# Kernel tuning notes

Measured on AMD Instinct MI355X. Metric: run time of the kernel, lower is better.

The kernel has to match this reference:

```python
import jax, jax.numpy as jnp
import numpy as np

N_NODES = 50000
N_EDGES = 1600000
IN_FEATS = 256
OUT_FEATS = 64


def setup_inputs() -> dict:
    key = jax.random.key(0)
    k_x, k_w, k_b, k_s, k_d = jax.random.split(key, 5)
    x = jax.random.normal(k_x, (N_NODES, IN_FEATS), dtype=jnp.float32)
    # nn.Linear(in_feats, out_feats): weight [out, in], bias [out]
    W = jax.random.normal(k_w, (OUT_FEATS, IN_FEATS), dtype=jnp.float32) / np.sqrt(IN_FEATS)
    b = jax.random.normal(k_b, (OUT_FEATS,), dtype=jnp.float32) * 0.01
    edge_src = jax.random.randint(k_s, (N_EDGES,), 0, N_NODES, dtype=jnp.int32)
    edge_dst = jax.random.randint(k_d, (N_EDGES,), 0, N_NODES, dtype=jnp.int32)
    return {"x": x, "W": W, "b": b, "edge_src": edge_src, "edge_dst": edge_dst}


def reference(x, W, b, edge_src, edge_dst):
    # h = dropout(relu(Linear(x)))  -- dropout p=0 (eval) => identity
    h = jax.nn.relu(x @ W.T + b)                     # [N, out_feats]
    # update_all: message = h[src], reduce = mean over incoming edges per dst
    msg = h[edge_src]                                # [E, out_feats] gather
    summed = jax.ops.segment_sum(msg, edge_dst, num_segments=N_NODES)  # [N, out]
    deg = jax.ops.segment_sum(jnp.ones((edge_src.shape[0],), dtype=h.dtype),
                              edge_dst, num_segments=N_NODES)          # [N]
    deg = jnp.maximum(deg, 1.0)
    return summed / deg[:, None]
```

## Files before the change

### kernel.cpp

```cpp
#include <hip/hip_runtime.h>
#include <hip/hip_bf16.h>

#define K_IN 256
#define O_OUT 64
#define NBINS 1024
#define NPB 49
#define CAP 1824
#define PART_CHUNK 4096
#define WS_STRIDE 264
#define XS_STRIDE 136

typedef __attribute__((ext_vector_type(8))) short short8;
typedef __attribute__((ext_vector_type(4))) float f32x4;

__device__ inline unsigned short bf16bits(float a) {
  __hip_bfloat16 t = __float2bfloat16(a);
  return *(unsigned short*)&t;
}

__global__ __launch_bounds__(256) void k_prep(const float* __restrict__ W,
                                              unsigned short* __restrict__ Wb,
                                              int* __restrict__ cursor) {
  int i = blockIdx.x * 256 + threadIdx.x;
  Wb[i] = bf16bits(W[i]);
  if (i < NBINS) cursor[i] = 0;
}

__global__ __launch_bounds__(256) void k_gemm_mfma(const float* __restrict__ x,
                                                   const unsigned short* __restrict__ Wb,
                                                   const float* __restrict__ bias,
                                                   __hip_bfloat16* __restrict__ h,
                                                   int N) {
  __shared__ unsigned short wsb[64 * WS_STRIDE];
  __shared__ unsigned short xs[64 * XS_STRIDE];

  const int tid = threadIdx.x;
  const int lane = tid & 63;
  const int wv = tid >> 6;
  const int n0 = blockIdx.x * 64;

  {
    const unsigned* wsrc = (const unsigned*)Wb;
    unsigned* wdst = (unsigned*)wsb;
#pragma unroll
    for (int r = 0; r < 32; ++r) {
      int flat = r * 256 + tid;
      int row = flat >> 7;
      int col = flat & 127;
      wdst[row * (WS_STRIDE / 2) + col] = wsrc[flat];
    }
  }

  f32x4 acc[4] = {{0.f, 0.f, 0.f, 0.f}, {0.f, 0.f, 0.f, 0.f},
                  {0.f, 0.f, 0.f, 0.f}, {0.f, 0.f, 0.f, 0.f}};

  for (int kc = 0; kc < K_IN; kc += 128) {
    __syncthreads();
    unsigned* xdst = (unsigned*)xs;
#pragma unroll
    for (int r = 0; r < 8; ++r) {
      int flat = r * 256 + tid;
      int row = flat >> 5;
      int c4 = flat & 31;
      float4 v = make_float4(0.f, 0.f, 0.f, 0.f);
      int node = n0 + row;
      if (node < N) v = *(const float4*)(x + (size_t)node * K_IN + kc + c4 * 4);
      unsigned u0 = (unsigned)bf16bits(v.x) | ((unsigned)bf16bits(v.y) << 16);
      unsigned u1 = (unsigned)bf16bits(v.z) | ((unsigned)bf16bits(v.w) << 16);
      xdst[row * (XS_STRIDE / 2) + c4 * 2] = u0;
      xdst[row * (XS_STRIDE / 2) + c4 * 2 + 1] = u1;
    }
    __syncthreads();

    const unsigned short* arow =
        xs + (wv * 16 + (lane & 15)) * XS_STRIDE + (lane >> 4) * 8;
    const unsigned short* bcol =
        wsb + (lane & 15) * WS_STRIDE + kc + (lane >> 4) * 8;
#pragma unroll
    for (int k0 = 0; k0 < 128; k0 += 32) {
      short8 a = *(const short8*)(arow + k0);
#pragma unroll
      for (int nt = 0; nt < 4; ++nt) {
        short8 bfr = *(const short8*)(bcol + nt * 16 * WS_STRIDE + k0);
        acc[nt] = __builtin_amdgcn_mfma_f32_16x16x32_bf16(a, bfr, acc[nt], 0, 0, 0);
      }
    }
  }

  const int col = lane & 15;
  const int rbase = (lane >> 4) * 4;
#pragma unroll
  for (int nt = 0; nt < 4; ++nt) {
    float bv = bias[nt * 16 + col];
#pragma unroll
    for (int j = 0; j < 4; ++j) {
      int node = n0 + wv * 16 + rbase + j;
      if (node < N) {
        float v = fmaxf(acc[nt][j] + bv, 0.f);
        h[(size_t)node * O_OUT + nt * 16 + col] = __float2bfloat16(v);
      }
    }
  }
}

__global__ __launch_bounds__(256) void k_part(const int* __restrict__ esrc,
                                              const int* __restrict__ edst,
                                              int* __restrict__ cursor,
                                              unsigned* __restrict__ bucket, int E) {
  __shared__ int cnt[NBINS];
  __shared__ int scanb[NBINS];
  __shared__ int gbase[NBINS];
  __shared__ int wsum[4];
  __shared__ unsigned ord[PART_CHUNK];
  __shared__ unsigned short obin[PART_CHUNK];

  const int tid = threadIdx.x;
  const int lane = tid & 63;
  const int wid = tid >> 6;
  const int base = blockIdx.x * PART_CHUNK;

#pragma unroll
  for (int r = 0; r < 4; ++r) cnt[r * 256 + tid] = 0;
  __syncthreads();

  unsigned pk[16];
  int bn[16];
  int rk[16];
#pragma unroll
  for (int r = 0; r < 4; ++r) {
    int e0 = base + r * 1024 + tid * 4;
    int4 s4, d4;
    if (e0 + 3 < E) {
      s4 = *(const int4*)(esrc + e0);
      d4 = *(const int4*)(edst + e0);
    } else {
      s4 = make_int4(0, 0, 0, 0);
      d4 = make_int4(0, 0, 0, 0);
      int* sp = (int*)&s4;
      int* dp = (int*)&d4;
      for (int j = 0; j < 4; ++j)
        if (e0 + j < E) { sp[j] = esrc[e0 + j]; dp[j] = edst[e0 + j]; }
    }
    const int* sp = (const int*)&s4;
    const int* dp = (const int*)&d4;
#pragma unroll
    for (int j = 0; j < 4; ++j) {
      int k = r * 4 + j;
      int e = e0 + j;
      if (e < E) {
        int s = sp[j];
        int d = dp[j];
        int bb = (int)__umulhi((unsigned)d, 87652394u);
        int dl = d - bb * NPB;
        pk[k] = (unsigned)s | ((unsigned)dl << 16);
        bn[k] = bb;
        rk[k] = atomicAdd(&cnt[bb], 1);
      } else {
        bn[k] = -1;
      }
    }
  }
  __syncthreads();

  int c0 = cnt[4 * tid];
  int c1 = cnt[4 * tid + 1];
  int c2 = cnt[4 * tid + 2];
  int c3 = cnt[4 * tid + 3];
  int s = c0 + c1 + c2 + c3;
  int incl = s;
#pragma unroll
  for (int off = 1; off < 64; off <<= 1) {
    int t = __shfl_up(incl, off);
    if (lane >= off) incl += t;
  }
  if (lane == 63) wsum[wid] = incl;
  __syncthreads();
  int wpre = 0;
  for (int w = 0; w < wid; ++w) wpre += wsum[w];
  int excl = wpre + incl - s;
  scanb[4 * tid] = excl;
  scanb[4 * tid + 1] = excl + c0;
  scanb[4 * tid + 2] = excl + c0 + c1;
  scanb[4 * tid + 3] = excl + c0 + c1 + c2;
  gbase[4 * tid] = (c0 > 0) ? atomicAdd(&cursor[4 * tid], c0) : 0;
  gbase[4 * tid + 1] = (c1 > 0) ? atomicAdd(&cursor[4 * tid + 1], c1) : 0;
  gbase[4 * tid + 2] = (c2 > 0) ? atomicAdd(&cursor[4 * tid + 2], c2) : 0;
  gbase[4 * tid + 3] = (c3 > 0) ? atomicAdd(&cursor[4 * tid + 3], c3) : 0;
  __syncthreads();

#pragma unroll
  for (int k = 0; k < 16; ++k) {
    if (bn[k] >= 0) {
      int pos = scanb[bn[k]] + rk[k];
      ord[pos] = pk[k];
      obin[pos] = (unsigned short)bn[k];
    }
  }
  __syncthreads();

  int nv = E - base;
  if (nv > PART_CHUNK) nv = PART_CHUNK;
  for (int p = tid; p < nv; p += 256) {
    int bb = obin[p];
    int slot = gbase[bb] + (p - scanb[bb]);
    if (slot < CAP) bucket[(size_t)bb * CAP + slot] = ord[p];
  }
}

__global__ __launch_bounds__(512) void k_sortagg(const unsigned* __restrict__ bucket,
                                                 const int* __restrict__ cursor,
                                                 const unsigned* __restrict__ h32,
                                                 float* __restrict__ out, int N) {
  __shared__ int hist[NPB];
  __shared__ int offs[NPB];
  __shared__ unsigned short sbuf[CAP];

  const int tid = threadIdx.x;
  const int lane = tid & 63;
  const int wid = tid >> 6;
  const int bin = blockIdx.x;

  if (tid < NPB) hist[tid] = 0;
  __syncthreads();

  int cnt = cursor[bin];
  if (cnt > CAP) cnt = CAP;
  const unsigned* bb = bucket + (size_t)bin * CAP;

  unsigned pk[4];
  int rk[4];
  {
    int i0 = tid * 4;
    uint4 v;
    if (i0 + 3 < cnt) {
      v = *(const uint4*)(bb + i0);
    } else {
      v = make_uint4(0, 0, 0, 0);
      unsigned* vp = (unsigned*)&v;
      for (int j = 0; j < 4; ++j)
        if (i0 + j < cnt) vp[j] = bb[i0 + j];
    }
    const unsigned* vp = (const unsigned*)&v;
#pragma unroll
    for (int j = 0; j < 4; ++j) {
      if (i0 + j < cnt) {
        pk[j] = vp[j];
        rk[j] = atomicAdd(&hist[vp[j] >> 16], 1);
      } else {
        rk[j] = -1;
      }
    }
  }
  __syncthreads();

  if (tid < 64) {
    int hval = (tid < NPB) ? hist[tid] : 0;
    int incl = hval;
#pragma unroll
    for (int off = 1; off < 64; off <<= 1) {
      int t = __shfl_up(incl, off);
      if (lane >= off) incl += t;
    }
    if (tid < NPB) offs[tid] = incl - hval;
  }
  __syncthreads();

#pragma unroll
  for (int j = 0; j < 4; ++j) {
    if (rk[j] >= 0) sbuf[offs[pk[j] >> 16] + rk[j]] = (unsigned short)(pk[j] & 0xFFFFu);
  }
  __syncthreads();

  const int half = lane >> 5;
  const int hl = lane & 31;
  for (int nl = wid; nl < NPB; nl += 8) {
    int n = bin * NPB + nl;
    if (n >= N) break;
    int c = hist[nl];
    const unsigned short* bs = sbuf + offs[nl];

    float ax = 0.f, ay = 0.f;
    const int npairs = c >> 1;
    const int g8 = npairs & ~7;
    if (g8 > 0) {
      int p[8];
#pragma unroll
      for (int k = 0; k < 8; ++k) p[k] = bs[2 * k + half];
      for (int i = 8;; i += 8) {
        int q[8];
        bool more = (i < g8);
        if (more) {
#pragma unroll
          for (int k = 0; k < 8; ++k) q[k] = bs[2 * (i + k) + half];
        }
#pragma unroll
        for (int k = 0; k < 8; ++k) {
          unsigned u = h32[(size_t)p[k] * 32 + hl];
          ax += __uint_as_float(u << 16);
          ay += __uint_as_float(u & 0xFFFF0000u);
        }
        if (!more) break;
#pragma unroll
        for (int k = 0; k < 8; ++k) p[k] = q[k];
      }
    }
    for (int j = g8; j < npairs; ++j) {
      int p = bs[2 * j + half];
      unsigned u = h32[(size_t)p * 32 + hl];
      ax += __uint_as_float(u << 16);
      ay += __uint_as_float(u & 0xFFFF0000u);
    }
    if (c & 1) {
      int p = bs[c - 1];
      if (half == 0) {
        unsigned u = h32[(size_t)p * 32 + hl];
        ax += __uint_as_float(u << 16);
        ay += __uint_as_float(u & 0xFFFF0000u);
      }
    }

    float bx = __shfl(ax, lane ^ 32);
    float by = __shfl(ay, lane ^ 32);
    if (half == 0) {
      float inv = 1.f / fmaxf((float)c, 1.f);
      float2 r;
      r.x = (ax + bx) * inv;
      r.y = (ay + by) * inv;
      ((float2*)out)[(size_t)n * 32 + hl] = r;
    }
  }
}

extern "C" void kernel_launch(void* const* d_in, const int* in_sizes, int n_in,
                              void* d_out, int out_size, void* d_ws, size_t ws_size,
                              hipStream_t stream) {
  const float* x = (const float*)d_in[0];
  const float* W = (const float*)d_in[1];
  const float* b = (const float*)d_in[2];
  const int* esrc = (const int*)d_in[3];
  const int* edst = (const int*)d_in[4];
  float* out = (float*)d_out;

  const int N = in_sizes[0] / K_IN;
  const int E = in_sizes[3];

  char* ws = (char*)d_ws;
  unsigned short* Wb = (unsigned short*)ws;
  __hip_bfloat16* h = (__hip_bfloat16*)(ws + 32768);
  size_t off = 32768 + (size_t)N * O_OUT * sizeof(__hip_bfloat16);
  int* cursor = (int*)(ws + off);
  off += NBINS * sizeof(int);
  unsigned* bucket = (unsigned*)(ws + off);

  k_prep<<<(K_IN * O_OUT) / 256, 256, 0, stream>>>(W, Wb, cursor);
  k_gemm_mfma<<<(N + 63) / 64, 256, 0, stream>>>(x, Wb, b, h, N);
  k_part<<<(E + PART_CHUNK - 1) / PART_CHUNK, 256, 0, stream>>>(esrc, edst, cursor, bucket, E);
  k_sortagg<<<NBINS, 512, 0, stream>>>(bucket, cursor, (const unsigned*)h, out, N);
}
```

Measured before the change: 176.9 us.

## Fuse GEMM and edge partition kernels into one interleaved launch

Merges the MFMA linear+ReLU kernel and the edge partitioning kernel into a single launch. Blocks are interleaved so that every third block does partitioning and the rest do GEMM tiles, with shared memory overlaid through a union. This removes one kernel launch boundary and lets the compute-bound GEMM overlap the memory/atomic-bound partition work. The cost is that partition blocks now reserve the larger GEMM shared-memory footprint, which may lower occupancy.

```diff
diff --git a/kernel.cpp b/kernel.cpp
--- a/kernel.cpp
+++ b/kernel.cpp
@@ -26,22 +26,35 @@
   if (i < NBINS) cursor[i] = 0;
 }
 
-__global__ __launch_bounds__(256) void k_gemm_mfma(const float* __restrict__ x,
-                                                   const unsigned short* __restrict__ Wb,
-                                                   const float* __restrict__ bias,
-                                                   __hip_bfloat16* __restrict__ h,
-                                                   int N) {
-  __shared__ unsigned short wsb[64 * WS_STRIDE];
-  __shared__ unsigned short xs[64 * XS_STRIDE];
-
+struct GemmSmem {
+  unsigned short wsb[64 * WS_STRIDE];
+  unsigned short xs[64 * XS_STRIDE];
+};
+struct PartSmem {
+  int cnt[NBINS];
+  int scanb[NBINS];
+  int gbase[NBINS];
+  int wsum[4];
+  unsigned ord[PART_CHUNK];
+  unsigned short obin[PART_CHUNK];
+};
+union FusedSmem {
+  GemmSmem g;
+  PartSmem p;
+};
+
+__device__ void gemm_body(GemmSmem& sm, int gid, const float* __restrict__ x,
+                          const unsigned short* __restrict__ Wb,
+                          const float* __restrict__ bias,
+                          __hip_bfloat16* __restrict__ h, int N) {
   const int tid = threadIdx.x;
   const int lane = tid & 63;
   const int wv = tid >> 6;
-  const int n0 = blockIdx.x * 64;
+  const int n0 = gid * 64;
 
   {
     const unsigned* wsrc = (const unsigned*)Wb;
-    unsigned* wdst = (unsigned*)wsb;
+    unsigned* wdst = (unsigned*)sm.wsb;
 #pragma unroll
     for (int r = 0; r < 32; ++r) {
       int flat = r * 256 + tid;
@@ -56,7 +69,7 @@
 
   for (int kc = 0; kc < K_IN; kc += 128) {
     __syncthreads();
-    unsigned* xdst = (unsigned*)xs;
+    unsigned* xdst = (unsigned*)sm.xs;
 #pragma unroll
     for (int r = 0; r < 8; ++r) {
       int flat = r * 256 + tid;
@@ -73,9 +86,9 @@
     __syncthreads();
 
     const unsigned short* arow =
-        xs + (wv * 16 + (lane & 15)) * XS_STRIDE + (lane >> 4) * 8;
+        sm.xs + (wv * 16 + (lane & 15)) * XS_STRIDE + (lane >> 4) * 8;
     const unsigned short* bcol =
-        wsb + (lane & 15) * WS_STRIDE + kc + (lane >> 4) * 8;
+        sm.wsb + (lane & 15) * WS_STRIDE + kc + (lane >> 4) * 8;
 #pragma unroll
     for (int k0 = 0; k0 < 128; k0 += 32) {
       short8 a = *(const short8*)(arow + k0);
@@ -103,24 +116,16 @@
   }
 }
 
-__global__ __launch_bounds__(256) void k_part(const int* __restrict__ esrc,
-                                              const int* __restrict__ edst,
-                                              int* __restrict__ cursor,
-                                              unsigned* __restrict__ bucket, int E) {
-  __shared__ int cnt[NBINS];
-  __shared__ int scanb[NBINS];
-  __shared__ int gbase[NBINS];
-  __shared__ int wsum[4];
-  __shared__ unsigned ord[PART_CHUNK];
-  __shared__ unsigned short obin[PART_CHUNK];
-
+__device__ void part_body(PartSmem& sm, int pid, const int* __restrict__ esrc,
+                          const int* __restrict__ edst, int* __restrict__ cursor,
+                          unsigned* __restrict__ bucket, int E) {
   const int tid = threadIdx.x;
   const int lane = tid & 63;
   const int wid = tid >> 6;
-  const int base = blockIdx.x * PART_CHUNK;
-
-#pragma unroll
-  for (int r = 0; r < 4; ++r) cnt[r * 256 + tid] = 0;
+  const int base = pid * PART_CHUNK;
+
+#pragma unroll
+  for (int r = 0; r < 4; ++r) sm.cnt[r * 256 + tid] = 0;
   __syncthreads();
 
   unsigned pk[16];
@@ -154,7 +159,7 @@
         int dl = d - bb * NPB;
         pk[k] = (unsigned)s | ((unsigned)dl << 16);
         bn[k] = bb;
-        rk[k] = atomicAdd(&cnt[bb], 1);
+        rk[k] = atomicAdd(&sm.cnt[bb], 1);
       } else {
         bn[k] = -1;
       }
@@ -162,10 +167,10 @@
   }
   __syncthreads();
 
-  int c0 = cnt[4 * tid];
-  int c1 = cnt[4 * tid + 1];
-  int c2 = cnt[4 * tid + 2];
-  int c3 = cnt[4 * tid + 3];
+  int c0 = sm.cnt[4 * tid];
+  int c1 = sm.cnt[4 * tid + 1];
+  int c2 = sm.cnt[4 * tid + 2];
+  int c3 = sm.cnt[4 * tid + 3];
   int s = c0 + c1 + c2 + c3;
   int incl = s;
 #pragma unroll
@@ -173,27 +178,27 @@
     int t = __shfl_up(incl, off);
     if (lane >= off) incl += t;
   }
-  if (lane == 63) wsum[wid] = incl;
+  if (lane == 63) sm.wsum[wid] = incl;
   __syncthreads();
   int wpre = 0;
-  for (int w = 0; w < wid; ++w) wpre += wsum[w];
+  for (int w = 0; w < wid; ++w) wpre += sm.wsum[w];
   int excl = wpre + incl - s;
-  scanb[4 * tid] = excl;
-  scanb[4 * tid + 1] = excl + c0;
-  scanb[4 * tid + 2] = excl + c0 + c1;
-  scanb[4 * tid + 3] = excl + c0 + c1 + c2;
-  gbase[4 * tid] = (c0 > 0) ? atomicAdd(&cursor[4 * tid], c0) : 0;
-  gbase[4 * tid + 1] = (c1 > 0) ? atomicAdd(&cursor[4 * tid + 1], c1) : 0;
-  gbase[4 * tid + 2] = (c2 > 0) ? atomicAdd(&cursor[4 * tid + 2], c2) : 0;
-  gbase[4 * tid + 3] = (c3 > 0) ? atomicAdd(&cursor[4 * tid + 3], c3) : 0;
+  sm.scanb[4 * tid] = excl;
+  sm.scanb[4 * tid + 1] = excl + c0;
+  sm.scanb[4 * tid + 2] = excl + c0 + c1;
+  sm.scanb[4 * tid + 3] = excl + c0 + c1 + c2;
+  sm.gbase[4 * tid] = (c0 > 0) ? atomicAdd(&cursor[4 * tid], c0) : 0;
+  sm.gbase[4 * tid + 1] = (c1 > 0) ? atomicAdd(&cursor[4 * tid + 1], c1) : 0;
+  sm.gbase[4 * tid + 2] = (c2 > 0) ? atomicAdd(&cursor[4 * tid + 2], c2) : 0;
+  sm.gbase[4 * tid + 3] = (c3 > 0) ? atomicAdd(&cursor[4 * tid + 3], c3) : 0;
   __syncthreads();
 
 #pragma unroll
   for (int k = 0; k < 16; ++k) {
     if (bn[k] >= 0) {
-      int pos = scanb[bn[k]] + rk[k];
-      ord[pos] = pk[k];
-      obin[pos] = (unsigned short)bn[k];
+      int pos = sm.scanb[bn[k]] + rk[k];
+      sm.ord[pos] = pk[k];
+      sm.obin[pos] = (unsigned short)bn[k];
     }
   }
   __syncthreads();
@@ -201,9 +206,30 @@
   int nv = E - base;
   if (nv > PART_CHUNK) nv = PART_CHUNK;
   for (int p = tid; p < nv; p += 256) {
-    int bb = obin[p];
-    int slot = gbase[bb] + (p - scanb[bb]);
-    if (slot < CAP) bucket[(size_t)bb * CAP + slot] = ord[p];
+    int bb = sm.obin[p];
+    int slot = sm.gbase[bb] + (p - sm.scanb[bb]);
+    if (slot < CAP) bucket[(size_t)bb * CAP + slot] = sm.ord[p];
+  }
+}
+
+__global__ __launch_bounds__(256) void k_fused(const float* __restrict__ x,
+                                               const unsigned short* __restrict__ Wb,
+                                               const float* __restrict__ bias,
+                                               __hip_bfloat16* __restrict__ h,
+                                               const int* __restrict__ esrc,
+                                               const int* __restrict__ edst,
+                                               int* __restrict__ cursor,
+                                               unsigned* __restrict__ bucket,
+                                               int N, int E) {
+  __shared__ FusedSmem sm;
+  const int npart = (E + PART_CHUNK - 1) / PART_CHUNK;
+  const int b = blockIdx.x;
+  if (b % 3 == 1 && b / 3 < npart) {
+    part_body(sm.p, b / 3, esrc, edst, cursor, bucket, E);
+  } else {
+    int skipped = (b + 2) / 3;
+    if (skipped > npart) skipped = npart;
+    gemm_body(sm.g, b - skipped, x, Wb, bias, h, N);
   }
 }
 
@@ -352,8 +378,11 @@
   off += NBINS * sizeof(int);
   unsigned* bucket = (unsigned*)(ws + off);
 
+  const int ngemm = (N + 63) / 64;
+  const int npart = (E + PART_CHUNK - 1) / PART_CHUNK;
+
   k_prep<<<(K_IN * O_OUT) / 256, 256, 0, stream>>>(W, Wb, cursor);
-  k_gemm_mfma<<<(N + 63) / 64, 256, 0, stream>>>(x, Wb, b, h, N);
-  k_part<<<(E + PART_CHUNK - 1) / PART_CHUNK, 256, 0, stream>>>(esrc, edst, cursor, bucket, E);
+  k_fused<<<ngemm + npart, 256, 0, stream>>>(x, Wb, b, h, esrc, edst, cursor,
+                                             bucket, N, E);
   k_sortagg<<<NBINS, 512, 0, stream>>>(bucket, cursor, (const unsigned*)h, out, N);
 }
```

Result: faster. 165.4 us (-6.5%).
